# Kernel tuning notes

Measured on AMD Instinct MI355X. Metric: run time of the kernel, lower is better.

## Reference

```python
import jax, jax.numpy as jnp
import numpy as np
from jax import lax

NUM_GROUP = 2048
GROUP_SIZE = 16


def setup_inputs() -> dict:
    key = jax.random.key(0)
    pcd = jax.random.normal(key, (4, 16384, 3), dtype=jnp.float32)
    return {"pcd": pcd}


def _fps(xyz, n_samples):
    # Furthest point sampling, matching CUDA FPS: start at index 0,
    # iteratively pick the point with max min-distance to the chosen set.
    B, N, _ = xyz.shape

    def step(carry, _):
        min_d, last = carry
        p = jnp.take_along_axis(xyz, last[:, None, None], axis=1)  # B,1,3
        d = jnp.sum((xyz - p) ** 2, axis=-1)                       # B,N
        min_d = jnp.minimum(min_d, d)
        nxt = jnp.argmax(min_d, axis=-1).astype(jnp.int32)         # B
        return (min_d, nxt), nxt

    first = jnp.zeros((B,), jnp.int32)
    init = (jnp.full((B, N), 1e10, xyz.dtype), first)
    _, rest = lax.scan(step, init, None, length=n_samples - 1)     # (n-1),B
    return jnp.concatenate([first[None, :], rest], axis=0).T       # B,n


def reference(pcd):
    xyz = pcd                                                      # channel==3 path
    B, N, _ = xyz.shape
    # centers via FPS + gather (N != num_group branch)
    fps_idx = _fps(xyz, NUM_GROUP)                                 # B,G
    center = jnp.take_along_axis(xyz, fps_idx[:, :, None], axis=1) # B,G,3
    # kNN of each center among all points (squared L2)
    d2 = (jnp.sum(center * center, -1)[:, :, None]
          - 2.0 * jnp.einsum('bgc,bnc->bgn', center, xyz)
          + jnp.sum(xyz * xyz, -1)[:, None, :])                    # B,G,N
    _, idx = lax.top_k(-d2, GROUP_SIZE)                            # B,G,M (nearest first)
    # gather neighborhoods per batch
    nbr = jax.vmap(lambda x, i: x[i])(xyz, idx)                    # B,G,M,3
    neighborhood = nbr - center[:, :, None, :]
    return neighborhood, center
```

## Files before the change

kernel.cpp:

```cpp
#include <hip/hip_runtime.h>
#include <math.h>


#pragma clang fp contract(off)

#define N_PTS 16384
#define N_GROUP 2048
#define GROUP_SIZE 16
#define FPS_THREADS 512
#define NPAIR 16
#define FPS_WAVES (FPS_THREADS / 64)
#define KNN_THREADS 256
#define KNN_WAVES (KNN_THREADS / 64)

__device__ __forceinline__ float fmul_sep(float a, float b) {
  float r = a * b;
  asm volatile("" : "+v"(r));
  return r;
}

__device__ __forceinline__ unsigned long long shfl_xor_u64(unsigned long long v, int off) {
  const unsigned int lo = __shfl_xor((unsigned int)v, off);
  const unsigned int hi = __shfl_xor((unsigned int)(v >> 32), off);
  return ((unsigned long long)hi << 32) | lo;
}

__device__ __forceinline__ float2 pk_add(float2 a, float2 b) {
  float2 d;
  asm("v_pk_add_f32 %0, %1, %2" : "=v"(d) : "v"(a), "v"(b));
  return d;
}
__device__ __forceinline__ float2 pk_sq(float2 a) {
  float2 d;
  asm("v_pk_mul_f32 %0, %1, %1" : "=v"(d) : "v"(a));
  return d;
}

__global__ __launch_bounds__(FPS_THREADS)
__attribute__((amdgpu_waves_per_eu(2, 2)))
void fps_kernel(const float* __restrict__ pcd, float* __restrict__ center) {
#pragma clang fp contract(off)
  const int b = blockIdx.x;
  const int t = threadIdx.x;
  const int lane = t & 63;
  const int wid = t >> 6;
  const float* xyz = pcd + (size_t)b * N_PTS * 3;

  __shared__ float2 XP[NPAIR * FPS_THREADS];
  __shared__ float2 YP[NPAIR * FPS_THREADS];
  __shared__ unsigned long long skey[2][FPS_WAVES];
  __shared__ float sx[2][FPS_WAVES], sy[2][FPS_WAVES], sz[2][FPS_WAVES];

  float2 Z[NPAIR], MD[NPAIR];
#pragma unroll
  for (int j = 0; j < NPAIR; ++j) {
    const int i0 = (2 * j) * FPS_THREADS + t;
    const int i1 = i0 + FPS_THREADS;
    XP[j * FPS_THREADS + t] = make_float2(xyz[i0 * 3 + 0], xyz[i1 * 3 + 0]);
    YP[j * FPS_THREADS + t] = make_float2(xyz[i0 * 3 + 1], xyz[i1 * 3 + 1]);
    Z[j] = make_float2(xyz[i0 * 3 + 2], xyz[i1 * 3 + 2]);
    MD[j] = make_float2(1e10f, 1e10f);
  }
#pragma unroll
  for (int j = 0; j < NPAIR; ++j) asm("" : "+v"(Z[j]));

  float px = xyz[0], py = xyz[1], pz = xyz[2];
  if (t == 0) {
    center[((size_t)b * N_GROUP) * 3 + 0] = px;
    center[((size_t)b * N_GROUP) * 3 + 1] = py;
    center[((size_t)b * N_GROUP) * 3 + 2] = pz;
  }
  __syncthreads();

  for (int it = 1; it < N_GROUP; ++it) {
    const int p = it & 1;
    const float2 npx2 = make_float2(-px, -px);
    const float2 npy2 = make_float2(-py, -py);
    const float2 npz2 = make_float2(-pz, -pz);
    float bv = -1.0f;
#pragma unroll
    for (int j = 0; j < NPAIR; ++j) {
      const float2 dx = pk_add(XP[j * FPS_THREADS + t], npx2);
      const float2 dy = pk_add(YP[j * FPS_THREADS + t], npy2);
      const float2 dz = pk_add(Z[j], npz2);
      const float2 sxq = pk_sq(dx);
      const float2 syq = pk_sq(dy);
      const float2 szq = pk_sq(dz);
      const float2 s = pk_add(pk_add(sxq, syq), szq);
      MD[j].x = fminf(MD[j].x, s.x);
      MD[j].y = fminf(MD[j].y, s.y);
      bv = fmaxf(bv, MD[j].x);
      bv = fmaxf(bv, MD[j].y);
    }
    int ii = 0;
#pragma unroll
    for (int j = NPAIR - 1; j >= 0; --j) {
      if (MD[j].y == bv) ii = 2 * j + 1;
      if (MD[j].x == bv) ii = 2 * j;
    }
    const int bi = ii * FPS_THREADS + t;
    unsigned long long key =
        ((unsigned long long)__float_as_uint(bv) << 32) |
        (unsigned int)(N_PTS - 1 - bi);

#pragma unroll
    for (int off = 32; off > 0; off >>= 1) {
      const unsigned long long ok = shfl_xor_u64(key, off);
      if (ok > key) key = ok;
    }
    if (lane == 0) {
      const int kidx = N_PTS - 1 - (int)(unsigned int)(key & 0xffffffffu);
      skey[p][wid] = key;
      sx[p][wid] = xyz[kidx * 3 + 0];
      sy[p][wid] = xyz[kidx * 3 + 1];
      sz[p][wid] = xyz[kidx * 3 + 2];
    }
    __syncthreads();
    unsigned long long bk = skey[p][0];
    int bj = 0;
#pragma unroll
    for (int j = 1; j < FPS_WAVES; ++j) {
      const unsigned long long kj = skey[p][j];
      if (kj > bk) { bk = kj; bj = j; }
    }
    px = sx[p][bj]; py = sy[p][bj]; pz = sz[p][bj];
    if (t == 0) {
      center[((size_t)b * N_GROUP + it) * 3 + 0] = px;
      center[((size_t)b * N_GROUP + it) * 3 + 1] = py;
      center[((size_t)b * N_GROUP + it) * 3 + 2] = pz;
    }
  }
}

__global__ __launch_bounds__(KNN_THREADS) void knn_kernel(
    const float* __restrict__ pcd, const float* __restrict__ center,
    float* __restrict__ nbr) {
#pragma clang fp contract(off)
  const int lane = threadIdx.x & 63;
  const int gw = blockIdx.x * KNN_WAVES + (threadIdx.x >> 6);
  const int b = gw >> 11;
  const float* xyz = pcd + (size_t)b * N_PTS * 3;

  const float c0 = center[(size_t)gw * 3 + 0];
  const float c1 = center[(size_t)gw * 3 + 1];
  const float c2 = center[(size_t)gw * 3 + 2];
  const float cc = (fmul_sep(c0, c0) + fmul_sep(c1, c1)) + fmul_sep(c2, c2);

  float lval = INFINITY;
  int lidx = 0;
  float worst = INFINITY;

  for (int ch = 0; ch < N_PTS / 64; ++ch) {
    const int n = ch * 64 + lane;
    const float xp = xyz[n * 3 + 0];
    const float yp = xyz[n * 3 + 1];
    const float zp = xyz[n * 3 + 2];
    const float xx = (fmul_sep(xp, xp) + fmul_sep(yp, yp)) + fmul_sep(zp, zp);
    const float dot = fmaf(c2, zp, fmaf(c1, yp, c0 * xp));
    const float d2 = (cc - fmul_sep(2.0f, dot)) + xx;

    unsigned long long m = __ballot(d2 < worst);
    while (m) {
      const int srcl = __ffsll((unsigned long long)m) - 1;
      m &= (m - 1);
      const float nv = __shfl(d2, srcl);
      if (nv < worst) {
        const int ni = ch * 64 + srcl;
        const int rank = __popcll(__ballot(lane < GROUP_SIZE && lval <= nv));
        const float shv = __shfl_up(lval, 1);
        const int   shi = __shfl_up(lidx, 1);
        if (lane < GROUP_SIZE) {
          if (lane == rank)      { lval = nv;  lidx = ni;  }
          else if (lane > rank)  { lval = shv; lidx = shi; }
        }
        worst = __shfl(lval, 15);
      }
    }
  }

  if (lane < GROUP_SIZE) {
    const float ox = xyz[lidx * 3 + 0] - c0;
    const float oy = xyz[lidx * 3 + 1] - c1;
    const float oz = xyz[lidx * 3 + 2] - c2;
    const size_t o = ((size_t)gw * GROUP_SIZE + lane) * 3;
    nbr[o + 0] = ox; nbr[o + 1] = oy; nbr[o + 2] = oz;
  }
}

extern "C" void kernel_launch(void* const* d_in, const int* in_sizes, int n_in,
                              void* d_out, int out_size, void* d_ws, size_t ws_size,
                              hipStream_t stream) {
  const float* pcd = (const float*)d_in[0];
  const int B = in_sizes[0] / (N_PTS * 3);

  float* out = (float*)d_out;
  float* nbr = out;
  float* center = out + (size_t)B * N_GROUP * GROUP_SIZE * 3;

  fps_kernel<<<B, FPS_THREADS, 0, stream>>>(pcd, center);
  knn_kernel<<<(B * N_GROUP) / KNN_WAVES, KNN_THREADS, 0, stream>>>(pcd, center, nbr);
}
```

Measured before the change: 4.476 ms.

## Use contiguous per-thread point layout and float argmax reduction in FPS

Each thread now owns 32 contiguous points, so a point's index order matches thread and slot order. This lets the per-wave argmax use a float-max shuffle reduction plus a ballot/ffs tie-break in place of 64-bit key shuffles. The winning point's z comes from registers and its x/y from shared memory, replacing global-memory reloads of the chosen point each iteration. The change adds strided global loads at init and relies on the lowest lane being the lowest index for ties.

```diff
diff --git a/kernel.cpp b/kernel.cpp
--- a/kernel.cpp
+++ b/kernel.cpp
@@ -17,12 +17,6 @@
   float r = a * b;
   asm volatile("" : "+v"(r));
   return r;
-}
-
-__device__ __forceinline__ unsigned long long shfl_xor_u64(unsigned long long v, int off) {
-  const unsigned int lo = __shfl_xor((unsigned int)v, off);
-  const unsigned int hi = __shfl_xor((unsigned int)(v >> 32), off);
-  return ((unsigned long long)hi << 32) | lo;
 }
 
 __device__ __forceinline__ float2 pk_add(float2 a, float2 b) {
@@ -48,17 +42,15 @@
 
   __shared__ float2 XP[NPAIR * FPS_THREADS];
   __shared__ float2 YP[NPAIR * FPS_THREADS];
-  __shared__ unsigned long long skey[2][FPS_WAVES];
-  __shared__ float sx[2][FPS_WAVES], sy[2][FPS_WAVES], sz[2][FPS_WAVES];
+  __shared__ float4 sres[2][FPS_WAVES];
 
   float2 Z[NPAIR], MD[NPAIR];
 #pragma unroll
   for (int j = 0; j < NPAIR; ++j) {
-    const int i0 = (2 * j) * FPS_THREADS + t;
-    const int i1 = i0 + FPS_THREADS;
-    XP[j * FPS_THREADS + t] = make_float2(xyz[i0 * 3 + 0], xyz[i1 * 3 + 0]);
-    YP[j * FPS_THREADS + t] = make_float2(xyz[i0 * 3 + 1], xyz[i1 * 3 + 1]);
-    Z[j] = make_float2(xyz[i0 * 3 + 2], xyz[i1 * 3 + 2]);
+    const int i0 = t * 32 + 2 * j;
+    XP[j * FPS_THREADS + t] = make_float2(xyz[i0 * 3 + 0], xyz[i0 * 3 + 3]);
+    YP[j * FPS_THREADS + t] = make_float2(xyz[i0 * 3 + 1], xyz[i0 * 3 + 4]);
+    Z[j] = make_float2(xyz[i0 * 3 + 2], xyz[i0 * 3 + 5]);
     MD[j] = make_float2(1e10f, 1e10f);
   }
 #pragma unroll
@@ -83,47 +75,48 @@
       const float2 dx = pk_add(XP[j * FPS_THREADS + t], npx2);
       const float2 dy = pk_add(YP[j * FPS_THREADS + t], npy2);
       const float2 dz = pk_add(Z[j], npz2);
-      const float2 sxq = pk_sq(dx);
-      const float2 syq = pk_sq(dy);
-      const float2 szq = pk_sq(dz);
-      const float2 s = pk_add(pk_add(sxq, syq), szq);
+      const float2 s = pk_add(pk_add(pk_sq(dx), pk_sq(dy)), pk_sq(dz));
       MD[j].x = fminf(MD[j].x, s.x);
       MD[j].y = fminf(MD[j].y, s.y);
       bv = fmaxf(bv, MD[j].x);
       bv = fmaxf(bv, MD[j].y);
     }
+
     int ii = 0;
+    float zw = Z[0].x;
 #pragma unroll
     for (int j = NPAIR - 1; j >= 0; --j) {
-      if (MD[j].y == bv) ii = 2 * j + 1;
-      if (MD[j].x == bv) ii = 2 * j;
+      if (MD[j].y == bv) { ii = 2 * j + 1; zw = Z[j].y; }
+      if (MD[j].x == bv) { ii = 2 * j;     zw = Z[j].x; }
     }
-    const int bi = ii * FPS_THREADS + t;
-    unsigned long long key =
-        ((unsigned long long)__float_as_uint(bv) << 32) |
-        (unsigned int)(N_PTS - 1 - bi);
 
+    float wm = bv;
 #pragma unroll
-    for (int off = 32; off > 0; off >>= 1) {
-      const unsigned long long ok = shfl_xor_u64(key, off);
-      if (ok > key) key = ok;
-    }
-    if (lane == 0) {
-      const int kidx = N_PTS - 1 - (int)(unsigned int)(key & 0xffffffffu);
-      skey[p][wid] = key;
-      sx[p][wid] = xyz[kidx * 3 + 0];
-      sy[p][wid] = xyz[kidx * 3 + 1];
-      sz[p][wid] = xyz[kidx * 3 + 2];
-    }
+    for (int off = 32; off > 0; off >>= 1) wm = fmaxf(wm, __shfl_xor(wm, off));
+
+    const unsigned long long mask = __ballot(bv == wm);
+    const int wl = __ffsll(mask) - 1;
+    const int widx = (wid * 64 + wl) * 32 + __shfl(ii, wl);
+    const float wz = __shfl(zw, wl);
+    if (lane == 0)
+      sres[p][wid] = make_float4(wm, wz, __int_as_float(widx), 0.0f);
     __syncthreads();
-    unsigned long long bk = skey[p][0];
-    int bj = 0;
+
+    float4 r0 = sres[p][0];
+    float bb = r0.x; int bw = 0;
 #pragma unroll
     for (int j = 1; j < FPS_WAVES; ++j) {
-      const unsigned long long kj = skey[p][j];
-      if (kj > bk) { bk = kj; bj = j; }
+      const float vj = sres[p][j].x;
+      if (vj > bb) { bb = vj; bw = j; }
     }
-    px = sx[p][bj]; py = sy[p][bj]; pz = sz[p][bj];
+    const float4 win = sres[p][bw];
+    const int idx = __float_as_int(win.z);
+    pz = win.y;
+    const int tw = idx >> 5, iw = idx & 31, jw = iw >> 1, k = iw & 1;
+    const float2 qx = XP[jw * FPS_THREADS + tw];
+    const float2 qy = YP[jw * FPS_THREADS + tw];
+    px = k ? qx.y : qx.x;
+    py = k ? qy.y : qy.x;
     if (t == 0) {
       center[((size_t)b * N_GROUP + it) * 3 + 0] = px;
       center[((size_t)b * N_GROUP + it) * 3 + 1] = py;
```

Result: slower. 4.593 ms (+2.6%).

## Spatially bin points into tiles and prune FPS updates with bounding-box bounds

Applied to the files above, without the earlier changes.

The FPS kernel now sorts points into an 8x8x8 grid via histogram and prefix scan, and stores them in tiles of 32 in workspace memory along with per-tile bounding boxes. The main loop runs on a single wave. Each iteration skips tiles whose box lower-bound distance cannot beat the tile's current max min-distance. Tie-breaking by original index is encoded into 64-bit keys, and the wave-level reduction removes the block-wide barrier per iteration. The trade-offs are a setup cost, loss of parallelism from using one wave, and global-memory reads for active tiles.

```diff
diff --git a/kernel.cpp b/kernel.cpp
--- a/kernel.cpp
+++ b/kernel.cpp
@@ -7,11 +7,14 @@
 #define N_PTS 16384
 #define N_GROUP 2048
 #define GROUP_SIZE 16
-#define FPS_THREADS 512
-#define NPAIR 16
-#define FPS_WAVES (FPS_THREADS / 64)
+#define SETUP_THREADS 512
+#define NTILE 512
+#define NSLOT 8
+#define NPAIRT 16
+#define NCELL 512
 #define KNN_THREADS 256
 #define KNN_WAVES (KNN_THREADS / 64)
+#define WS_PER_BATCH (16384 * 3 + 16384 * 4)
 
 __device__ __forceinline__ float fmul_sep(float a, float b) {
   float r = a * b;
@@ -24,7 +27,10 @@
   const unsigned int hi = __shfl_xor((unsigned int)(v >> 32), off);
   return ((unsigned long long)hi << 32) | lo;
 }
-
+__device__ __forceinline__ unsigned long long maxu64(unsigned long long a,
+                                                     unsigned long long b) {
+  return a > b ? a : b;
+}
 __device__ __forceinline__ float2 pk_add(float2 a, float2 b) {
   float2 d;
   asm("v_pk_add_f32 %0, %1, %2" : "=v"(d) : "v"(a), "v"(b));
@@ -36,95 +42,214 @@
   return d;
 }
 
-__global__ __launch_bounds__(FPS_THREADS)
-__attribute__((amdgpu_waves_per_eu(2, 2)))
-void fps_kernel(const float* __restrict__ pcd, float* __restrict__ center) {
+__device__ __forceinline__ int cell_coord(float v, float mn, float s) {
+  int c = (int)((v - mn) * s);
+  return c < 0 ? 0 : (c > 7 ? 7 : c);
+}
+
+__global__ __launch_bounds__(SETUP_THREADS) void fps_kernel(
+    const float* __restrict__ pcd, float* __restrict__ center,
+    float* __restrict__ ws) {
 #pragma clang fp contract(off)
   const int b = blockIdx.x;
   const int t = threadIdx.x;
   const int lane = t & 63;
   const int wid = t >> 6;
   const float* xyz = pcd + (size_t)b * N_PTS * 3;
-
-  __shared__ float2 XP[NPAIR * FPS_THREADS];
-  __shared__ float2 YP[NPAIR * FPS_THREADS];
-  __shared__ unsigned long long skey[2][FPS_WAVES];
-  __shared__ float sx[2][FPS_WAVES], sy[2][FPS_WAVES], sz[2][FPS_WAVES];
-
-  float2 Z[NPAIR], MD[NPAIR];
-#pragma unroll
-  for (int j = 0; j < NPAIR; ++j) {
-    const int i0 = (2 * j) * FPS_THREADS + t;
-    const int i1 = i0 + FPS_THREADS;
-    XP[j * FPS_THREADS + t] = make_float2(xyz[i0 * 3 + 0], xyz[i1 * 3 + 0]);
-    YP[j * FPS_THREADS + t] = make_float2(xyz[i0 * 3 + 1], xyz[i1 * 3 + 1]);
-    Z[j] = make_float2(xyz[i0 * 3 + 2], xyz[i1 * 3 + 2]);
-    MD[j] = make_float2(1e10f, 1e10f);
-  }
-#pragma unroll
-  for (int j = 0; j < NPAIR; ++j) asm("" : "+v"(Z[j]));
+  float* wsx = ws + (size_t)b * WS_PER_BATCH;
+  float* wsy = wsx + 16384;
+  float* wsz = wsy + 16384;
+  float* ws4 = wsz + 16384;
+
+  __shared__ float2 md2[NPAIRT * NTILE];
+  __shared__ unsigned short oidx16[N_PTS];
+  __shared__ int hist[NCELL], base_[NCELL], cnt[NCELL];
+  __shared__ int scanA[NCELL], scanB[NCELL];
+  __shared__ float bb6[6];
+  __shared__ float wred[8][6];
+
+  hist[t] = 0; cnt[t] = 0;
+  float mnx = 1e30f, mny = 1e30f, mnz = 1e30f;
+  float mxx = -1e30f, mxy = -1e30f, mxz = -1e30f;
+  for (int i = 0; i < 32; ++i) {
+    const int idx = t * 32 + i;
+    const float x = xyz[idx * 3 + 0];
+    const float y = xyz[idx * 3 + 1];
+    const float z = xyz[idx * 3 + 2];
+    mnx = fminf(mnx, x); mxx = fmaxf(mxx, x);
+    mny = fminf(mny, y); mxy = fmaxf(mxy, y);
+    mnz = fminf(mnz, z); mxz = fmaxf(mxz, z);
+  }
+#pragma unroll
+  for (int off = 32; off > 0; off >>= 1) {
+    mnx = fminf(mnx, __shfl_xor(mnx, off)); mxx = fmaxf(mxx, __shfl_xor(mxx, off));
+    mny = fminf(mny, __shfl_xor(mny, off)); mxy = fmaxf(mxy, __shfl_xor(mxy, off));
+    mnz = fminf(mnz, __shfl_xor(mnz, off)); mxz = fmaxf(mxz, __shfl_xor(mxz, off));
+  }
+  if (lane == 0) {
+    wred[wid][0] = mnx; wred[wid][1] = mny; wred[wid][2] = mnz;
+    wred[wid][3] = mxx; wred[wid][4] = mxy; wred[wid][5] = mxz;
+  }
+  __syncthreads();
+  if (t == 0) {
+    float a0 = wred[0][0], a1 = wred[0][1], a2 = wred[0][2];
+    float a3 = wred[0][3], a4 = wred[0][4], a5 = wred[0][5];
+    for (int j = 1; j < 8; ++j) {
+      a0 = fminf(a0, wred[j][0]); a1 = fminf(a1, wred[j][1]);
+      a2 = fminf(a2, wred[j][2]); a3 = fmaxf(a3, wred[j][3]);
+      a4 = fmaxf(a4, wred[j][4]); a5 = fmaxf(a5, wred[j][5]);
+    }
+    bb6[0] = a0; bb6[1] = a1; bb6[2] = a2;
+    bb6[3] = 8.0f / fmaxf(a3 - a0, 1e-30f);
+    bb6[4] = 8.0f / fmaxf(a4 - a1, 1e-30f);
+    bb6[5] = 8.0f / fmaxf(a5 - a2, 1e-30f);
+  }
+  __syncthreads();
+  const float c_mnx = bb6[0], c_mny = bb6[1], c_mnz = bb6[2];
+  const float c_sx = bb6[3], c_sy = bb6[4], c_sz = bb6[5];
+
+  for (int i = 0; i < 32; ++i) {
+    const int idx = t * 32 + i;
+    const int cx = cell_coord(xyz[idx * 3 + 0], c_mnx, c_sx);
+    const int cy = cell_coord(xyz[idx * 3 + 1], c_mny, c_sy);
+    const int cz = cell_coord(xyz[idx * 3 + 2], c_mnz, c_sz);
+    atomicAdd(&hist[(cx << 6) | (cy << 3) | cz], 1);
+  }
+  __syncthreads();
+  scanA[t] = hist[t];
+  __syncthreads();
+#pragma unroll
+  for (int step = 0; step < 9; ++step) {
+    const int off = 1 << step;
+    int* src = (step & 1) ? scanB : scanA;
+    int* dst = (step & 1) ? scanA : scanB;
+    const int v = src[t] + (t >= off ? src[t - off] : 0);
+    dst[t] = v;
+    __syncthreads();
+  }
+  base_[t] = scanB[t] - hist[t];
+  __syncthreads();
+  for (int i = 0; i < 32; ++i) {
+    const int idx = t * 32 + i;
+    const float x = xyz[idx * 3 + 0];
+    const float y = xyz[idx * 3 + 1];
+    const float z = xyz[idx * 3 + 2];
+    const int cx = cell_coord(x, c_mnx, c_sx);
+    const int cy = cell_coord(y, c_mny, c_sy);
+    const int cz = cell_coord(z, c_mnz, c_sz);
+    const int c = (cx << 6) | (cy << 3) | cz;
+    const int pos = base_[c] + atomicAdd(&cnt[c], 1);
+    const int tile = pos >> 5, w = pos & 31, k = w >> 1, comp = w & 1;
+    wsx[(k * NTILE + tile) * 2 + comp] = x;
+    wsy[(k * NTILE + tile) * 2 + comp] = y;
+    wsz[(k * NTILE + tile) * 2 + comp] = z;
+    ws4[pos * 4 + 0] = x; ws4[pos * 4 + 1] = y; ws4[pos * 4 + 2] = z;
+    oidx16[(k * NTILE + tile) * 2 + comp] = (unsigned short)idx;
+  }
+#pragma unroll
+  for (int j = 0; j < NPAIRT; ++j) md2[j * NTILE + t] = make_float2(1e10f, 1e10f);
+  __threadfence_block();
+  __syncthreads();
+  if (wid != 0) return;
+
+  const float2* wx2 = (const float2*)wsx;
+  const float2* wy2 = (const float2*)wsy;
+  const float2* wz2 = (const float2*)wsz;
+  const unsigned* op32 = (const unsigned*)oidx16;
+  const unsigned long long V1E10 = (unsigned long long)__float_as_uint(1e10f) << 32;
+
+  float bxl[NSLOT], bxh[NSLOT], byl[NSLOT], byh[NSLOT], bzl[NSLOT], bzh[NSLOT];
+  unsigned long long tkey[NSLOT];
+#pragma unroll
+  for (int s = 0; s < NSLOT; ++s) {
+    const int tile = s * 64 + lane;
+    float l0 = 1e30f, l1 = 1e30f, l2 = 1e30f, h0 = -1e30f, h1 = -1e30f, h2 = -1e30f;
+    unsigned long long nk = 0;
+    for (int k = 0; k < NPAIRT; ++k) {
+      const float2 X = wx2[k * NTILE + tile];
+      const float2 Y = wy2[k * NTILE + tile];
+      const float2 Z = wz2[k * NTILE + tile];
+      l0 = fminf(l0, fminf(X.x, X.y)); h0 = fmaxf(h0, fmaxf(X.x, X.y));
+      l1 = fminf(l1, fminf(Y.x, Y.y)); h1 = fmaxf(h1, fmaxf(Y.x, Y.y));
+      l2 = fminf(l2, fminf(Z.x, Z.y)); h2 = fmaxf(h2, fmaxf(Z.x, Z.y));
+      const unsigned op = op32[k * NTILE + tile];
+      const unsigned long long k0 =
+          V1E10 | ((unsigned long long)((16383u - (op & 0xffffu)) << 14)) |
+          (unsigned)(tile * 32 + 2 * k);
+      const unsigned long long k1 =
+          V1E10 | ((unsigned long long)((16383u - (op >> 16)) << 14)) |
+          (unsigned)(tile * 32 + 2 * k + 1);
+      nk = maxu64(nk, maxu64(k0, k1));
+    }
+    bxl[s] = l0; bxh[s] = h0; byl[s] = l1; byh[s] = h1; bzl[s] = l2; bzh[s] = h2;
+    tkey[s] = nk;
+    asm("" : "+v"(bxl[s]), "+v"(bxh[s]), "+v"(byl[s]), "+v"(byh[s]),
+              "+v"(bzl[s]), "+v"(bzh[s]));
+  }
 
   float px = xyz[0], py = xyz[1], pz = xyz[2];
-  if (t == 0) {
+  if (lane == 0) {
     center[((size_t)b * N_GROUP) * 3 + 0] = px;
     center[((size_t)b * N_GROUP) * 3 + 1] = py;
     center[((size_t)b * N_GROUP) * 3 + 2] = pz;
   }
-  __syncthreads();
+  const float4* w4 = (const float4*)ws4;
 
   for (int it = 1; it < N_GROUP; ++it) {
-    const int p = it & 1;
     const float2 npx2 = make_float2(-px, -px);
     const float2 npy2 = make_float2(-py, -py);
     const float2 npz2 = make_float2(-pz, -pz);
-    float bv = -1.0f;
-#pragma unroll
-    for (int j = 0; j < NPAIR; ++j) {
-      const float2 dx = pk_add(XP[j * FPS_THREADS + t], npx2);
-      const float2 dy = pk_add(YP[j * FPS_THREADS + t], npy2);
-      const float2 dz = pk_add(Z[j], npz2);
-      const float2 sxq = pk_sq(dx);
-      const float2 syq = pk_sq(dy);
-      const float2 szq = pk_sq(dz);
-      const float2 s = pk_add(pk_add(sxq, syq), szq);
-      MD[j].x = fminf(MD[j].x, s.x);
-      MD[j].y = fminf(MD[j].y, s.y);
-      bv = fmaxf(bv, MD[j].x);
-      bv = fmaxf(bv, MD[j].y);
-    }
-    int ii = 0;
-#pragma unroll
-    for (int j = NPAIR - 1; j >= 0; --j) {
-      if (MD[j].y == bv) ii = 2 * j + 1;
-      if (MD[j].x == bv) ii = 2 * j;
-    }
-    const int bi = ii * FPS_THREADS + t;
-    unsigned long long key =
-        ((unsigned long long)__float_as_uint(bv) << 32) |
-        (unsigned int)(N_PTS - 1 - bi);
-
-#pragma unroll
-    for (int off = 32; off > 0; off >>= 1) {
-      const unsigned long long ok = shfl_xor_u64(key, off);
-      if (ok > key) key = ok;
-    }
+#pragma unroll
+    for (int s = 0; s < NSLOT; ++s) {
+      const int tile = s * 64 + lane;
+      const float U = __uint_as_float((unsigned)(tkey[s] >> 32));
+      const float ddx = fmaxf(fmaxf(bxl[s] - px, px - bxh[s]), 0.0f);
+      const float ddy = fmaxf(fmaxf(byl[s] - py, py - byh[s]), 0.0f);
+      const float ddz = fmaxf(fmaxf(bzl[s] - pz, pz - bzh[s]), 0.0f);
+      const float pd = ((ddx * ddx) + (ddy * ddy)) + (ddz * ddz);
+      const bool act = pd < U * 1.001f;
+      if (__ballot(act)) {
+        if (act) {
+          unsigned long long nk = 0;
+#pragma unroll 4
+          for (int k = 0; k < NPAIRT; ++k) {
+            const float2 X = wx2[k * NTILE + tile];
+            const float2 Y = wy2[k * NTILE + tile];
+            const float2 Z = wz2[k * NTILE + tile];
+            float2 M = md2[k * NTILE + tile];
+            const float2 dX = pk_add(X, npx2);
+            const float2 dY = pk_add(Y, npy2);
+            const float2 dZ = pk_add(Z, npz2);
+            const float2 s2 = pk_add(pk_add(pk_sq(dX), pk_sq(dY)), pk_sq(dZ));
+            M.x = fminf(M.x, s2.x);
+            M.y = fminf(M.y, s2.y);
+            md2[k * NTILE + tile] = M;
+            const unsigned op = op32[k * NTILE + tile];
+            const unsigned long long k0 =
+                ((unsigned long long)__float_as_uint(M.x) << 32) |
+                ((unsigned long long)((16383u - (op & 0xffffu)) << 14)) |
+                (unsigned)(tile * 32 + 2 * k);
+            const unsigned long long k1 =
+                ((unsigned long long)__float_as_uint(M.y) << 32) |
+                ((unsigned long long)((16383u - (op >> 16)) << 14)) |
+                (unsigned)(tile * 32 + 2 * k + 1);
+            nk = maxu64(nk, maxu64(k0, k1));
+          }
+          tkey[s] = nk;
+        }
+      }
+    }
+    unsigned long long w01 = maxu64(tkey[0], tkey[1]);
+    unsigned long long w23 = maxu64(tkey[2], tkey[3]);
+    unsigned long long w45 = maxu64(tkey[4], tkey[5]);
+    unsigned long long w67 = maxu64(tkey[6], tkey[7]);
+    unsigned long long w = maxu64(maxu64(w01, w23), maxu64(w45, w67));
+#pragma unroll
+    for (int off = 32; off > 0; off >>= 1) w = maxu64(w, shfl_xor_u64(w, off));
+    const int pos = (int)(w & 0x3fffull);
+    const float4 pw = w4[pos];
+    px = pw.x; py = pw.y; pz = pw.z;
     if (lane == 0) {
-      const int kidx = N_PTS - 1 - (int)(unsigned int)(key & 0xffffffffu);
-      skey[p][wid] = key;
-      sx[p][wid] = xyz[kidx * 3 + 0];
-      sy[p][wid] = xyz[kidx * 3 + 1];
-      sz[p][wid] = xyz[kidx * 3 + 2];
-    }
-    __syncthreads();
-    unsigned long long bk = skey[p][0];
-    int bj = 0;
-#pragma unroll
-    for (int j = 1; j < FPS_WAVES; ++j) {
-      const unsigned long long kj = skey[p][j];
-      if (kj > bk) { bk = kj; bj = j; }
-    }
-    px = sx[p][bj]; py = sy[p][bj]; pz = sz[p][bj];
-    if (t == 0) {
       center[((size_t)b * N_GROUP + it) * 3 + 0] = px;
       center[((size_t)b * N_GROUP + it) * 3 + 1] = py;
       center[((size_t)b * N_GROUP + it) * 3 + 2] = pz;
@@ -197,6 +322,6 @@
   float* nbr = out;
   float* center = out + (size_t)B * N_GROUP * GROUP_SIZE * 3;
 
-  fps_kernel<<<B, FPS_THREADS, 0, stream>>>(pcd, center);
+  fps_kernel<<<B, SETUP_THREADS, 0, stream>>>(pcd, center, (float*)d_ws);
   knn_kernel<<<(B * N_GROUP) / KNN_WAVES, KNN_THREADS, 0, stream>>>(pcd, center, nbr);
 }
```

After: 16.66 ms. 3.72x slower.
